# Optimization experiments

Hardware: AMD Instinct MI355X
Metric: run time of the kernel (lower is better)

Reference implementation:

```python
import jax, jax.numpy as jnp
import numpy as np

IN, OUT, N = 4096, 4096, 8192

def setup_inputs() -> dict:
    key = jax.random.key(0)
    k = jax.random.split(key, 7)
    sigma_start = 1.0  # log_sigma init = log(1.0) = 0; we use small randn instead for generality
    return {
        "x": jax.random.normal(k[0], (N, IN), dtype=jnp.float32),
        "mu_weight": jax.random.normal(k[1], (OUT, IN), dtype=jnp.float32) * 0.02,
        "log_sigma_weight": jax.random.normal(k[2], (OUT, IN), dtype=jnp.float32) * 0.1 - 3.0,
        "mu_bias": jax.random.normal(k[3], (OUT,), dtype=jnp.float32) * 0.02,
        "log_sigma_bias": jax.random.normal(k[4], (OUT,), dtype=jnp.float32) * 0.1 - 3.0,
        "eps_w": jax.random.normal(k[5], (OUT, IN), dtype=jnp.float32),
        "eps_b": jax.random.normal(k[6], (OUT,), dtype=jnp.float32),
    }

def reference(x, mu_weight, log_sigma_weight, mu_bias, log_sigma_bias, eps_w, eps_b):
    # Reparameterized Gaussian weight sampling: W = mu + exp(log_sigma) * eps
    weight = mu_weight + jnp.exp(log_sigma_weight) * eps_w        # [OUT, IN]
    bias = mu_bias + jnp.exp(log_sigma_bias) * eps_b              # [OUT]
    # F.linear(x, W, b) = x @ W^T + b
    return jnp.einsum("ni,oi->no", x, weight) + bias               # [N, OUT]
```

## Files before the change

kernel.cpp:

```cpp
#include <hip/hip_runtime.h>
#include <hip/hip_bf16.h>
#include <stdint.h>


constexpr int M    = 8192;
constexpr int K    = 4096;
constexpr int NOUT = 4096;

typedef __bf16 bf16x8 __attribute__((ext_vector_type(8)));
typedef float  f32x4  __attribute__((ext_vector_type(4)));
typedef short  short8 __attribute__((ext_vector_type(8)));

#define DI __device__ __forceinline__

DI void gl_lds16(const void* g, void* l) {
  __builtin_amdgcn_global_load_lds(
      (__attribute__((address_space(1))) void*)(g),
      (__attribute__((address_space(3))) void*)(l),
      16, 0, 0);
}

union BF8 {
  __hip_bfloat16 h[8];
  short8 s;
};

constexpr int XBLK = (M * K / 8) / 256;
constexpr int WBLK = (NOUT * K / 8) / 256;
constexpr int BBLK = (NOUT + 255) / 256;

__global__ __launch_bounds__(256) void prep_kernel(
    const float* __restrict__ x, short* __restrict__ xb,
    const float* __restrict__ mu, const float* __restrict__ ls,
    const float* __restrict__ eps, short* __restrict__ wb,
    const float* __restrict__ mu_b, const float* __restrict__ ls_b,
    const float* __restrict__ eps_b, float* __restrict__ bias) {
  const int b = blockIdx.x;
  if (b < XBLK) {
    int i = b * 256 + threadIdx.x;
    const float4* src = (const float4*)x;
    float4 f0 = src[2 * i + 0];
    float4 f1 = src[2 * i + 1];
    BF8 u;
    u.h[0] = __float2bfloat16(f0.x);
    u.h[1] = __float2bfloat16(f0.y);
    u.h[2] = __float2bfloat16(f0.z);
    u.h[3] = __float2bfloat16(f0.w);
    u.h[4] = __float2bfloat16(f1.x);
    u.h[5] = __float2bfloat16(f1.y);
    u.h[6] = __float2bfloat16(f1.z);
    u.h[7] = __float2bfloat16(f1.w);
    ((short8*)xb)[i] = u.s;
  } else if (b < XBLK + WBLK) {
    int i = (b - XBLK) * 256 + threadIdx.x;
    const float4* mu4 = (const float4*)mu;
    const float4* ls4 = (const float4*)ls;
    const float4* ep4 = (const float4*)eps;
    float4 m0 = mu4[2 * i + 0], m1 = mu4[2 * i + 1];
    float4 l0 = ls4[2 * i + 0], l1 = ls4[2 * i + 1];
    float4 e0 = ep4[2 * i + 0], e1 = ep4[2 * i + 1];
    BF8 u;
    u.h[0] = __float2bfloat16(m0.x + __expf(l0.x) * e0.x);
    u.h[1] = __float2bfloat16(m0.y + __expf(l0.y) * e0.y);
    u.h[2] = __float2bfloat16(m0.z + __expf(l0.z) * e0.z);
    u.h[3] = __float2bfloat16(m0.w + __expf(l0.w) * e0.w);
    u.h[4] = __float2bfloat16(m1.x + __expf(l1.x) * e1.x);
    u.h[5] = __float2bfloat16(m1.y + __expf(l1.y) * e1.y);
    u.h[6] = __float2bfloat16(m1.z + __expf(l1.z) * e1.z);
    u.h[7] = __float2bfloat16(m1.w + __expf(l1.w) * e1.w);
    ((short8*)wb)[i] = u.s;
  } else {
    int i = (b - XBLK - WBLK) * 256 + threadIdx.x;
    if (i < NOUT) bias[i] = mu_b[i] + expf(ls_b[i]) * eps_b[i];
  }
}

constexpr int BM = 256, BN = 256, BK = 32;
constexpr int NT = K / BK;

__global__ __launch_bounds__(512, 2) void gemm_bt_kernel(const short* __restrict__ A,
                                                         const short* __restrict__ B,
                                                         const float* __restrict__ bias,
                                                         float* __restrict__ C) {
  __shared__ __align__(16) short Alds[4][BM * BK];
  __shared__ __align__(16) short Blds[4][BN * BK];

  const int tid  = threadIdx.x;
  const int lane = tid & 63;
  const int wave = tid >> 6;
  const int wm   = wave >> 2;
  const int wn   = wave & 3;
  const int mrow = lane & 15;
  const int quad = lane >> 4;

  const int bid = blockIdx.x;
  const int swz = (bid & 7) * 64 + (bid >> 3);
  const int m0  = (swz >> 4) * BM;
  const int n0  = (swz & 15) * BN;

  const int c0 = tid, c1 = 512 + tid;
  const int cb0 = (wave << 6);
  const int cb1 = 512 + (wave << 6);
  const int r0 = c0 >> 2, r1 = c1 >> 2;
  const int sl0 = (c0 & 3) ^ ((r0 >> 1) & 3);
  const int sl1 = (c1 & 3) ^ ((r1 >> 1) & 3);
  const short* gA0 = A + (size_t)(m0 + r0) * K + sl0 * 8;
  const short* gA1 = A + (size_t)(m0 + r1) * K + sl1 * 8;
  const short* gB0 = B + (size_t)(n0 + r0) * K + sl0 * 8;
  const short* gB1 = B + (size_t)(n0 + r1) * K + sl1 * 8;

  const int slot = quad ^ ((mrow >> 1) & 3);
  const int aOff = (wm * 128 + mrow) * 64 + slot * 16;
  const int bOff = (wn * 64 + mrow) * 64 + slot * 16;

  f32x4 acc[8][4] = {};
  bf16x8 bfr[4];

#define PH0(tt, DOSTAGE)                                                    \
  do {                                                                      \
    const char* _Ab = (const char*)Alds[(tt) & 3] + aOff;                   \
    const char* _Bb = (const char*)Blds[(tt) & 3] + bOff;                   \
    bf16x8 afr[4];                                                          \
    _Pragma("unroll") for (int mi = 0; mi < 4; ++mi)                        \
        afr[mi] = *(const bf16x8*)(_Ab + mi * 1024);                        \
    _Pragma("unroll") for (int ni = 0; ni < 4; ++ni)                        \
        bfr[ni] = *(const bf16x8*)(_Bb + ni * 1024);                        \
    if (DOSTAGE) {                                                          \
      const int _b = ((tt) + 3) & 3;                                        \
      const int _k = ((tt) + 3) * BK;                                       \
      gl_lds16(gA0 + _k, (char*)Alds[_b] + cb0 * 16);                       \
      gl_lds16(gB0 + _k, (char*)Blds[_b] + cb0 * 16);                       \
    }                                                                       \
    __builtin_amdgcn_s_barrier();                                           \
    __builtin_amdgcn_s_setprio(1);                                          \
    _Pragma("unroll") for (int mi = 0; mi < 4; ++mi)                        \
        _Pragma("unroll") for (int ni = 0; ni < 4; ++ni)                    \
            acc[mi][ni] = __builtin_amdgcn_mfma_f32_16x16x32_bf16(          \
                afr[mi], bfr[ni], acc[mi][ni], 0, 0, 0);                    \
    __builtin_amdgcn_s_setprio(0);                                          \
    __builtin_amdgcn_s_barrier();                                           \
  } while (0)

#define PH1(tt, DOSTAGE, VMSTR)                                             \
  do {                                                                      \
    const char* _Ab = (const char*)Alds[(tt) & 3] + aOff;                   \
    bf16x8 afr[4];                                                          \
    _Pragma("unroll") for (int mi = 0; mi < 4; ++mi)                        \
        afr[mi] = *(const bf16x8*)(_Ab + (4 + mi) * 1024);                  \
    if (DOSTAGE) {                                                          \
      const int _b = ((tt) + 3) & 3;                                        \
      const int _k = ((tt) + 3) * BK;                                       \
      gl_lds16(gA1 + _k, (char*)Alds[_b] + cb1 * 16);                       \
      gl_lds16(gB1 + _k, (char*)Blds[_b] + cb1 * 16);                       \
    }                                                                       \
    __builtin_amdgcn_s_barrier();                                           \
    __builtin_amdgcn_s_setprio(1);                                          \
    _Pragma("unroll") for (int mi = 0; mi < 4; ++mi)                        \
        _Pragma("unroll") for (int ni = 0; ni < 4; ++ni)                    \
            acc[4 + mi][ni] = __builtin_amdgcn_mfma_f32_16x16x32_bf16(      \
                afr[mi], bfr[ni], acc[4 + mi][ni], 0, 0, 0);                \
    __builtin_amdgcn_s_setprio(0);                                          \
    asm volatile("s_waitcnt vmcnt(" VMSTR ")" ::: "memory");                \
    __builtin_amdgcn_s_barrier();                                           \
  } while (0)

#define STAGE(tt)                                           \
  do {                                                      \
    const int _b = (tt) & 3;                                \
    const int _k = (tt) * BK;                               \
    gl_lds16(gA0 + _k, (char*)Alds[_b] + cb0 * 16);         \
    gl_lds16(gA1 + _k, (char*)Alds[_b] + cb1 * 16);         \
    gl_lds16(gB0 + _k, (char*)Blds[_b] + cb0 * 16);         \
    gl_lds16(gB1 + _k, (char*)Blds[_b] + cb1 * 16);         \
  } while (0)

  STAGE(0);
  STAGE(1);
  STAGE(2);
  asm volatile("s_waitcnt vmcnt(8)" ::: "memory");
  __builtin_amdgcn_s_barrier();

#pragma unroll 4
  for (int t = 0; t < NT - 3; ++t) {
    PH0(t, 1);
    PH1(t, 1, "8");
  }
  PH0(NT - 3, 0);
  PH1(NT - 3, 0, "4");
  PH0(NT - 2, 0);
  PH1(NT - 2, 0, "0");
  PH0(NT - 1, 0);
  PH1(NT - 1, 0, "0");

#undef PH0
#undef PH1
#undef STAGE

#pragma unroll
  for (int ni = 0; ni < 4; ++ni) {
    const int col  = n0 + wn * 64 + ni * 16 + mrow;
    const float bv = bias[col];
#pragma unroll
    for (int mi = 0; mi < 8; ++mi) {
      const int rowb = m0 + wm * 128 + mi * 16 + quad * 4;
#pragma unroll
      for (int r = 0; r < 4; ++r)
        C[(size_t)(rowb + r) * NOUT + col] = acc[mi][ni][r] + bv;
    }
  }
}

extern "C" void kernel_launch(void* const* d_in, const int* in_sizes, int n_in,
                              void* d_out, int out_size, void* d_ws, size_t ws_size,
                              hipStream_t stream) {
  const float* x    = (const float*)d_in[0];
  const float* mu_w = (const float*)d_in[1];
  const float* ls_w = (const float*)d_in[2];
  const float* mu_b = (const float*)d_in[3];
  const float* ls_b = (const float*)d_in[4];
  const float* ep_w = (const float*)d_in[5];
  const float* ep_b = (const float*)d_in[6];
  float* out = (float*)d_out;

  char* ws = (char*)d_ws;
  short* xb   = (short*)(ws);
  short* wb   = (short*)(ws + (size_t)M * K * 2);
  float* bias = (float*)(ws + (size_t)M * K * 2 + (size_t)NOUT * K * 2);

  prep_kernel<<<XBLK + WBLK + BBLK, 256, 0, stream>>>(x, xb, mu_w, ls_w, ep_w, wb,
                                                      mu_b, ls_b, ep_b, bias);

  gemm_bt_kernel<<<(M / BM) * (NOUT / BN), 512, 0, stream>>>(xb, wb, bias, out);
}
```

Baseline: 640.0 us.

## Restructure GEMM mainloop to BK=64 double-buffered half-tile pipeline with cross-tile MFMA overlap

Doubles the K-step to 64 and replaces the 4-stage BK=32 ring with a 2-buffer layout split into 128-row halves. Each tile is issued in four sub-phases that interleave LDS reads, async global-to-LDS loads of the next tile's halves, and MFMAs, and the previous tile's second-half MFMAs are deferred so they overlap the next tile's reads. The LDS swizzle is changed to an 8-slot XOR over 128-byte rows. The aim is fewer barriers per K, more MFMA work per sync, and better hiding of global load latency. The cost is more live fragment registers and a more intricate barrier and vmcnt schedule, which risks hazards and higher register pressure.

```diff
diff --git a/kernel.cpp b/kernel.cpp
--- a/kernel.cpp
+++ b/kernel.cpp
@@ -75,15 +75,15 @@
   }
 }
 
-constexpr int BM = 256, BN = 256, BK = 32;
+constexpr int BM = 256, BN = 256, BK = 64;
 constexpr int NT = K / BK;
 
 __global__ __launch_bounds__(512, 2) void gemm_bt_kernel(const short* __restrict__ A,
                                                          const short* __restrict__ B,
                                                          const float* __restrict__ bias,
                                                          float* __restrict__ C) {
-  __shared__ __align__(16) short Alds[4][BM * BK];
-  __shared__ __align__(16) short Blds[4][BN * BK];
+  __shared__ __align__(16) short Alds[2][2][128 * 64];
+  __shared__ __align__(16) short Blds[2][2][128 * 64];
 
   const int tid  = threadIdx.x;
   const int lane = tid & 63;
@@ -98,103 +98,125 @@
   const int m0  = (swz >> 4) * BM;
   const int n0  = (swz & 15) * BN;
 
-  const int c0 = tid, c1 = 512 + tid;
-  const int cb0 = (wave << 6);
-  const int cb1 = 512 + (wave << 6);
-  const int r0 = c0 >> 2, r1 = c1 >> 2;
-  const int sl0 = (c0 & 3) ^ ((r0 >> 1) & 3);
-  const int sl1 = (c1 & 3) ^ ((r1 >> 1) & 3);
-  const short* gA0 = A + (size_t)(m0 + r0) * K + sl0 * 8;
-  const short* gA1 = A + (size_t)(m0 + r1) * K + sl1 * 8;
-  const short* gB0 = B + (size_t)(n0 + r0) * K + sl0 * 8;
-  const short* gB1 = B + (size_t)(n0 + r1) * K + sl1 * 8;
-
-  const int slot = quad ^ ((mrow >> 1) & 3);
-  const int aOff = (wm * 128 + mrow) * 64 + slot * 16;
-  const int bOff = (wn * 64 + mrow) * 64 + slot * 16;
-
-  f32x4 acc[8][4] = {};
-  bf16x8 bfr[4];
-
-#define PH0(tt, DOSTAGE)                                                    \
-  do {                                                                      \
-    const char* _Ab = (const char*)Alds[(tt) & 3] + aOff;                   \
-    const char* _Bb = (const char*)Blds[(tt) & 3] + bOff;                   \
-    bf16x8 afr[4];                                                          \
-    _Pragma("unroll") for (int mi = 0; mi < 4; ++mi)                        \
-        afr[mi] = *(const bf16x8*)(_Ab + mi * 1024);                        \
-    _Pragma("unroll") for (int ni = 0; ni < 4; ++ni)                        \
-        bfr[ni] = *(const bf16x8*)(_Bb + ni * 1024);                        \
-    if (DOSTAGE) {                                                          \
-      const int _b = ((tt) + 3) & 3;                                        \
-      const int _k = ((tt) + 3) * BK;                                       \
-      gl_lds16(gA0 + _k, (char*)Alds[_b] + cb0 * 16);                       \
-      gl_lds16(gB0 + _k, (char*)Blds[_b] + cb0 * 16);                       \
-    }                                                                       \
-    __builtin_amdgcn_s_barrier();                                           \
-    __builtin_amdgcn_s_setprio(1);                                          \
-    _Pragma("unroll") for (int mi = 0; mi < 4; ++mi)                        \
-        _Pragma("unroll") for (int ni = 0; ni < 4; ++ni)                    \
-            acc[mi][ni] = __builtin_amdgcn_mfma_f32_16x16x32_bf16(          \
-                afr[mi], bfr[ni], acc[mi][ni], 0, 0, 0);                    \
-    __builtin_amdgcn_s_setprio(0);                                          \
-    __builtin_amdgcn_s_barrier();                                           \
-  } while (0)
-
-#define PH1(tt, DOSTAGE, VMSTR)                                             \
-  do {                                                                      \
-    const char* _Ab = (const char*)Alds[(tt) & 3] + aOff;                   \
-    bf16x8 afr[4];                                                          \
-    _Pragma("unroll") for (int mi = 0; mi < 4; ++mi)                        \
-        afr[mi] = *(const bf16x8*)(_Ab + (4 + mi) * 1024);                  \
-    if (DOSTAGE) {                                                          \
-      const int _b = ((tt) + 3) & 3;                                        \
-      const int _k = ((tt) + 3) * BK;                                       \
-      gl_lds16(gA1 + _k, (char*)Alds[_b] + cb1 * 16);                       \
-      gl_lds16(gB1 + _k, (char*)Blds[_b] + cb1 * 16);                       \
-    }                                                                       \
-    __builtin_amdgcn_s_barrier();                                           \
-    __builtin_amdgcn_s_setprio(1);                                          \
-    _Pragma("unroll") for (int mi = 0; mi < 4; ++mi)                        \
-        _Pragma("unroll") for (int ni = 0; ni < 4; ++ni)                    \
-            acc[4 + mi][ni] = __builtin_amdgcn_mfma_f32_16x16x32_bf16(      \
-                afr[mi], bfr[ni], acc[4 + mi][ni], 0, 0, 0);                \
-    __builtin_amdgcn_s_setprio(0);                                          \
-    asm volatile("s_waitcnt vmcnt(" VMSTR ")" ::: "memory");                \
-    __builtin_amdgcn_s_barrier();                                           \
-  } while (0)
-
-#define STAGE(tt)                                           \
-  do {                                                      \
-    const int _b = (tt) & 3;                                \
-    const int _k = (tt) * BK;                               \
-    gl_lds16(gA0 + _k, (char*)Alds[_b] + cb0 * 16);         \
-    gl_lds16(gA1 + _k, (char*)Alds[_b] + cb1 * 16);         \
-    gl_lds16(gB0 + _k, (char*)Blds[_b] + cb0 * 16);         \
-    gl_lds16(gB1 + _k, (char*)Blds[_b] + cb1 * 16);         \
-  } while (0)
-
-  STAGE(0);
-  STAGE(1);
-  STAGE(2);
+  const int    r0  = tid >> 3;
+  const int    kc0 = (tid & 7) ^ (r0 & 7);
+  const size_t offG = (size_t)r0 * K + kc0 * 8;
+  const short* pA0 = A + (size_t)m0 * K + offG;
+  const short* pA1 = pA0 + (size_t)64 * K;
+  const short* pB0 = B + (size_t)n0 * K + offG;
+  const short* pB1 = pB0 + (size_t)64 * K;
+  const int ldsOff0 = wave << 10;
+  const int ldsOff1 = 8192 + (wave << 10);
+
+  const int pk0   = quad ^ (mrow & 7);
+  const int aByte = mrow * 128 + pk0 * 16;
+  const int bByte = ((wn & 1) * 64 + mrow) * 128 + pk0 * 16;
+
+  f32x4  acc[8][4] = {};
+  bf16x8 aLo[8], aHi[8], bLo[4], bHi[4];
+
+#define STG_A(bufc, h, t)                                                      \
+  do {                                                                         \
+    gl_lds16(pA0 + (size_t)(h) * 128 * K + (t) * BK,                           \
+             (char*)&Alds[bufc][h][0] + ldsOff0);                              \
+    gl_lds16(pA1 + (size_t)(h) * 128 * K + (t) * BK,                           \
+             (char*)&Alds[bufc][h][0] + ldsOff1);                              \
+  } while (0)
+#define STG_B(bufc, h, t)                                                      \
+  do {                                                                         \
+    gl_lds16(pB0 + (size_t)(h) * 128 * K + (t) * BK,                           \
+             (char*)&Blds[bufc][h][0] + ldsOff0);                              \
+    gl_lds16(pB1 + (size_t)(h) * 128 * K + (t) * BK,                           \
+             (char*)&Blds[bufc][h][0] + ldsOff1);                              \
+  } while (0)
+
+#define RD_A(p, dst, mibase)                                                   \
+  do {                                                                         \
+    const char* Ah = (const char*)&Alds[p][wm][0];                             \
+    _Pragma("unroll") for (int mi = 0; mi < 4; ++mi) {                         \
+      dst[mi * 2 + 0] = *(const bf16x8*)(Ah + ((mibase) + mi) * 2048 + aByte); \
+      dst[mi * 2 + 1] =                                                        \
+          *(const bf16x8*)(Ah + ((mibase) + mi) * 2048 + (aByte ^ 64));        \
+    }                                                                          \
+  } while (0)
+#define RD_B(p, dst, nibase, cnt)                                              \
+  do {                                                                         \
+    const char* Bh = (const char*)&Blds[p][wn >> 1][0];                        \
+    _Pragma("unroll") for (int ni = 0; ni < (cnt); ++ni) {                     \
+      dst[ni * 2 + 0] = *(const bf16x8*)(Bh + ((nibase) + ni) * 2048 + bByte); \
+      dst[ni * 2 + 1] =                                                        \
+          *(const bf16x8*)(Bh + ((nibase) + ni) * 2048 + (bByte ^ 64));        \
+    }                                                                          \
+  } while (0)
+
+#define MM(mib, nib, afr, bfr)                                                 \
+  do {                                                                         \
+    __builtin_amdgcn_s_setprio(1);                                             \
+    _Pragma("unroll") for (int mi = 0; mi < 4; ++mi)                           \
+        _Pragma("unroll") for (int ni = 0; ni < 2; ++ni)                       \
+            _Pragma("unroll") for (int kk = 0; kk < 2; ++kk)                   \
+                acc[(mib) + mi][(nib) + ni] =                                  \
+                    __builtin_amdgcn_mfma_f32_16x16x32_bf16(                   \
+                        afr[mi * 2 + kk], bfr[ni * 2 + kk],                    \
+                        acc[(mib) + mi][(nib) + ni], 0, 0, 0);                 \
+    __builtin_amdgcn_s_setprio(0);                                             \
+  } while (0)
+
+#define BAR __builtin_amdgcn_s_barrier()
+
+#define TILE(p, MFPREV, S1OK, S2OK, VMSTR, tS)                                 \
+  do {                                                                         \
+                                                                       \
+    RD_A(p, aLo, 0);                                                           \
+    if (S1OK) STG_A(p ^ 1, 1, (tS) + 1);                                       \
+    BAR;                                                                       \
+    if (MFPREV) MM(4, 0, aHi, bLo);                                            \
+    BAR;                                                                       \
+                                                                       \
+    RD_B(p, bLo, 0, 2);                                                        \
+    if (S1OK) STG_B(p ^ 1, 0, (tS) + 1);                                       \
+    BAR;                                                                       \
+    if (MFPREV) MM(4, 2, aHi, bHi);                                            \
+    BAR;                                                                       \
+                                                            \
+    RD_B(p, bHi, 2, 2);                                                        \
+    RD_A(p, aHi, 4);                                                           \
+    if (S1OK) STG_B(p ^ 1, 1, (tS) + 1);                                       \
+    BAR;                                                                       \
+    MM(0, 0, aLo, bLo);                                                        \
+    BAR;                                                                       \
+                                                             \
+    if (S2OK) STG_A(p, 0, (tS) + 2);                                           \
+    BAR;                                                                       \
+    MM(0, 2, aLo, bHi);                                                        \
+    asm volatile("s_waitcnt vmcnt(" VMSTR ")" ::: "memory");                   \
+    BAR;                                                                       \
+  } while (0)
+
+  STG_A(0, 0, 0); STG_A(0, 1, 0); STG_B(0, 0, 0); STG_B(0, 1, 0);
+  STG_A(1, 0, 1); STG_A(1, 1, 1); STG_B(1, 0, 1); STG_B(1, 1, 1);
   asm volatile("s_waitcnt vmcnt(8)" ::: "memory");
-  __builtin_amdgcn_s_barrier();
-
-#pragma unroll 4
-  for (int t = 0; t < NT - 3; ++t) {
-    PH0(t, 1);
-    PH1(t, 1, "8");
+  BAR;
+
+  TILE(0, 0, 0, 1, "2", 0);
+  TILE(1, 1, 1, 1, "2", 1);
+#pragma unroll 1
+  for (int t = 2; t < NT - 2; t += 2) {
+    TILE(0, 1, 1, 1, "2", t);
+    TILE(1, 1, 1, 1, "2", t + 1);
   }
-  PH0(NT - 3, 0);
-  PH1(NT - 3, 0, "4");
-  PH0(NT - 2, 0);
-  PH1(NT - 2, 0, "0");
-  PH0(NT - 1, 0);
-  PH1(NT - 1, 0, "0");
-
-#undef PH0
-#undef PH1
-#undef STAGE
+  TILE(0, 1, 1, 0, "0", NT - 2);
+  TILE(1, 1, 0, 0, "0", NT - 1);
+  MM(4, 0, aHi, bLo);
+  MM(4, 2, aHi, bHi);
+
+#undef TILE
+#undef BAR
+#undef MM
+#undef RD_B
+#undef RD_A
+#undef STG_B
+#undef STG_A
 
 #pragma unroll
   for (int ni = 0; ni < 4; ++ni) {
```

After: 652.1 us. No clear change (+1.9%).
